# Performance work log

Hardware: AMD Instinct MI355X
Metric: run time of the kernel (lower is better)

The kernel has to match this reference:

```python
import jax, jax.numpy as jnp
import numpy as np

TOPK = 32
NUM_PT = 8192
NUM_KP = 8
HW = 19200


def _conv3(x, w, b):
    # x: [1, C, N], w: [O, C, 3] -> [1, O, N] (padding=1)
    y = jax.lax.conv_general_dilated(x, w, (1,), [(1, 1)],
                                     dimension_numbers=('NCH', 'OIH', 'NCH'))
    return y + b[None, :, None]


def setup_inputs() -> dict:
    key = jax.random.key(0)
    ks = jax.random.split(key, 64)

    def p(i, *shape):
        return (jax.random.normal(ks[i], shape, dtype=jnp.float32) * 0.05)

    inp = {
        'seg': jax.random.uniform(ks[0], (1, NUM_PT), dtype=jnp.float32),
        'img': jax.random.normal(ks[1], (1, 32, HW), dtype=jnp.float32),
        'cloud': jax.random.normal(ks[2], (1, NUM_PT, 3), dtype=jnp.float32),
        't': jax.random.normal(ks[3], (1, 3), dtype=jnp.float32),
        'choose': jax.random.randint(ks[4], (1, 1, NUM_PT), 0, HW),
        # Pseudo3DConv params (all 1x1 conv1d == channel matmul)
        'pconv1_w': p(5, 64, 3),    'pconv1_b': p(6, 64),
        'pconv2_w': p(7, 128, 64),  'pconv2_b': p(8, 128),
        'conv1_w': p(9, 64, 32),    'conv1_b': p(10, 64),
        'conv2_w': p(11, 128, 64),  'conv2_b': p(12, 128),
        'psconv1_w': p(13, 256, 128), 'psconv1_b': p(14, 256),
        'psconv2_w': p(15, 128, 256), 'psconv2_b': p(16, 128),
        'final_w': p(17, 128, 416), 'final_b': p(18, 128),
        # heads
        'seg1_w': p(19, 64, 128, 3), 'seg1_b': p(20, 64),
        'seg2_w': p(21, 32, 64),     'seg2_b': p(22, 32),
        'seg3_w': p(23, 1, 32),      'seg3_b': p(24, 1),
        'dis1_w': p(25, 64, 128, 3), 'dis1_b': p(26, 64),
        'dis2_w': p(27, 32, 64),     'dis2_b': p(28, 32),
        'dis3_w': p(29, 1, 32),      'dis3_b': p(30, 1),
        'lin1_w': p(31, 90, 128),    'lin1_b': p(32, 90),
        'lin2_w': p(33, 64, 90),     'lin2_b': p(34, 64),
        'lin3_w': p(35, 3 * NUM_KP, 64), 'lin3_b': p(36, 3 * NUM_KP),
    }
    return inp


def reference(seg, img, cloud, t, choose,
              pconv1_w, pconv1_b, pconv2_w, pconv2_b,
              conv1_w, conv1_b, conv2_w, conv2_b,
              psconv1_w, psconv1_b, psconv2_w, psconv2_b,
              final_w, final_b,
              seg1_w, seg1_b, seg2_w, seg2_b, seg3_w, seg3_b,
              dis1_w, dis1_b, dis2_w, dis2_b, dis3_w, dis3_b,
              lin1_w, lin1_b, lin2_w, lin2_b, lin3_w, lin3_b):
    lrelu = jax.nn.leaky_relu  # slope 0.01, same as torch default
    N = NUM_PT

    # gather per-point image features at chosen pixels: [N, 32]
    feat = jnp.take(img[0], choose[0, 0], axis=1).T
    c = cloud[0]  # [N, 3]

    # ---- KNN (self included, as in knn_cuda) ----
    d2 = jnp.sum((c[:, None, :] - c[None, :, :]) ** 2, axis=-1)  # [N, N]
    _, idx = jax.lax.top_k(-d2, TOPK)  # [N, K] nearest neighbors

    # ---- point-feature MLP (pconv1 -> lrelu -> pconv2) ----
    pf = lrelu(c @ pconv1_w.T + pconv1_b) @ pconv2_w.T + pconv2_b  # [N, 128]

    # ---- vectorized per-point neighbor gather + MLP + weighted maxpool ----
    nf = feat[idx]    # [N, K, 32]
    npf = pf[idx]     # [N, K, 128]
    npos = c[idx]     # [N, K, 3]
    w = jax.nn.softmax(-jnp.linalg.norm(c[:, None, :] - npos, axis=-1), axis=1)  # [N, K]

    f = lrelu(nf @ conv1_w.T + conv1_b) @ conv2_w.T + conv2_b          # [N, K, 128]
    fp = lrelu(npf @ psconv1_w.T + psconv1_b) @ psconv2_w.T + psconv2_b  # [N, K, 128]
    f = jnp.max(f * w[..., None], axis=1)    # [N, 128]
    fp = jnp.max(fp * w[..., None], axis=1)  # [N, 128]

    # final2 = [fp | img_feat], final1 = [f | cloud_feat] -> cat -> [N, 416]
    final = jnp.concatenate([fp, feat, f, pf], axis=1)
    fused = lrelu(final) @ final_w.T + final_b  # [N, 128]
    fused = fused.T[None]  # [1, 128, N]

    def pw(x, w_, b_):  # 1x1 conv1d on [1, C, N]
        return jnp.einsum('oc,bcn->bon', w_, x) + b_[None, :, None]

    # segmentation head
    h = lrelu(_conv3(fused, seg1_w, seg1_b))
    seg_pre = pw(lrelu(pw(h, seg2_w, seg2_b)), seg3_w, seg3_b).reshape(1, N)

    # distance-to-center weighting (norm along coord dim, softmax over points)
    dis_center = jax.nn.softmax(
        jnp.linalg.norm(cloud - (-t)[:, None, :], axis=2), axis=1)  # [1, N]

    # distance head (on unweighted fused features, matching torch op order)
    h = lrelu(_conv3(fused, dis1_w, dis1_b))
    dis_pre = pw(lrelu(pw(h, dis2_w, dis2_b)), dis3_w, dis3_b).reshape(1, N)

    # weight fused features by center distance and segmentation, sum-pool
    fused = fused * dis_center[:, None, :] * seg[:, None, :]
    g = jnp.sum(fused, axis=2)  # [1, 128]

    kp = lrelu(g @ lin1_w.T + lin1_b)
    kp = lrelu(kp @ lin2_w.T + lin2_b)
    keypoints = (kp @ lin3_w.T + lin3_b).reshape(1, NUM_KP, 3)
    return keypoints, dis_pre, dis_center, seg_pre
```

## Files before the change

### kernel.cpp

```cpp
#include <hip/hip_runtime.h>
#include <math.h>

#define NPT 8192
#define HWIMG 19200
#define KCAP 128

using short8 = __attribute__((ext_vector_type(8))) short;
using short4v = __attribute__((ext_vector_type(4))) short;
using f32x4  = __attribute__((ext_vector_type(4))) float;

__device__ __forceinline__ float lrelu(float x) { return x > 0.f ? x : 0.01f * x; }
__device__ __forceinline__ unsigned short f2bf(float v) {
  unsigned u = __float_as_uint(v);
  return (unsigned short)((u + 0x7fffu + ((u >> 16) & 1u)) >> 16);
}
__device__ __forceinline__ float bf2f(unsigned short h) {
  return __uint_as_float(((unsigned)h) << 16);
}
__device__ __forceinline__ void split2(float v, unsigned short& h, unsigned short& l) {
  h = f2bf(v);
  l = f2bf(v - bf2f(h));
}
__device__ __forceinline__ void mfma3(f32x4& acc, short8 ah, short8 al, short8 wh, short8 wl) {
  acc = __builtin_amdgcn_mfma_f32_16x16x32_bf16(ah, wh, acc, 0, 0, 0);
  acc = __builtin_amdgcn_mfma_f32_16x16x32_bf16(al, wh, acc, 0, 0, 0);
  acc = __builtin_amdgcn_mfma_f32_16x16x32_bf16(ah, wl, acc, 0, 0, 0);
}

__device__ __forceinline__ int swz(int o, int k, int Kc) {
  return ((((o >> 4) * Kc + (k >> 5)) << 6) + (((k >> 3) & 3) << 4) + (o & 15)) * 8 + (k & 7);
}

#define OFF_PCONV2  0
#define OFF_CONV1   8192
#define OFF_CONV2   10240
#define OFF_PSCONV1 18432
#define OFF_PSCONV2 51200
#define OFF_FINAL   83968
#define OFF_W3      137216
#define OFF_W2P     186368

#define S_C4    NPT
#define S_G     129
#define S_BIASC 128
#define S_B2C   64
#define S_FEAT  (NPT*32)
#define S_W3    49152
#define S_W2P   8192
#define S_WSPL  OFF_W3
#define PREP_TOTAL (S_C4 + S_G + S_BIASC + S_B2C + S_FEAT + S_W3 + S_W2P + S_WSPL)
__global__ void k_prep(const float* __restrict__ cloud, const int* __restrict__ choose,
                       const float* __restrict__ img,
                       const float* __restrict__ seg1_w, const float* __restrict__ dis1_w,
                       const float* __restrict__ seg1_b, const float* __restrict__ dis1_b,
                       const float* __restrict__ seg2_w, const float* __restrict__ dis2_w,
                       const float* __restrict__ seg2_b, const float* __restrict__ dis2_b,
                       const float* __restrict__ pconv2_w, const float* __restrict__ conv1_w,
                       const float* __restrict__ conv2_w, const float* __restrict__ psconv1_w,
                       const float* __restrict__ psconv2_w, const float* __restrict__ final_w,
                       float* __restrict__ c4, float* __restrict__ g,
                       float* __restrict__ biasc, float* __restrict__ bias2c,
                       float* __restrict__ feat,
                       unsigned short* __restrict__ feat_h, unsigned short* __restrict__ feat_l,
                       unsigned short* __restrict__ Wh, unsigned short* __restrict__ Wl) {
  int j = blockIdx.x * blockDim.x + threadIdx.x;
  if (j < S_C4) {
    float x = cloud[j*3+0], y = cloud[j*3+1], z = cloud[j*3+2];
    float4 v; v.x = x; v.y = y; v.z = z; v.w = x*x + y*y + z*z;
    ((float4*)c4)[j] = v;
    return;
  }
  j -= S_C4;
  if (j < S_G) { g[j] = 0.f; return; }
  j -= S_G;
  if (j < S_BIASC) { biasc[j] = (j < 64) ? seg1_b[j] : dis1_b[j-64]; return; }
  j -= S_BIASC;
  if (j < S_B2C) { bias2c[j] = (j < 32) ? seg2_b[j] : dis2_b[j-32]; return; }
  j -= S_B2C;
  if (j < S_FEAT) {
    int n = j >> 5, ch = j & 31;
    float v = img[ch*HWIMG + choose[n]];
    feat[j] = v;
    unsigned short hh, ll; split2(v, hh, ll);
    int d = swz(n, ch, 1);
    feat_h[d] = hh; feat_l[d] = ll;
    return;
  }
  j -= S_FEAT;
  if (j < S_W3) {
    int h = j / 24576, r = j - h*24576, o = r / 384, k = r - o*384;
    int t = k >> 7, c = k & 127;
    float v = (h ? dis1_w : seg1_w)[o*384 + c*3 + t];
    unsigned short hh, ll; split2(v, hh, ll);
    int d = OFF_W3 + swz(h*64 + o, k, 12);
    Wh[d] = hh; Wl[d] = ll;
    return;
  }
  j -= S_W3;
  if (j < S_W2P) {
    int o = j >> 7, c = j & 127;
    float v = 0.f;
    if (o < 32) { if (c < 64) v = seg2_w[o*64 + c]; }
    else        { if (c >= 64) v = dis2_w[(o-32)*64 + (c-64)]; }
    unsigned short hh, ll; split2(v, hh, ll);
    int d = OFF_W2P + swz(o, c, 4);
    Wh[d] = hh; Wl[d] = ll;
    return;
  }
  j -= S_W2P;
  if (j < S_WSPL) {
    float v; int d;
    if (j < OFF_CONV1) {
      int o = j >> 6, k = j & 63;
      v = pconv2_w[j]; d = OFF_PCONV2 + swz(o, k, 2);
    } else if (j < OFF_CONV2) {
      int jj = j - OFF_CONV1, o = jj >> 5, k = jj & 31;
      v = conv1_w[jj]; d = OFF_CONV1 + swz(o, k, 1);
    } else if (j < OFF_PSCONV1) {
      int jj = j - OFF_CONV2, o = jj >> 6, k = jj & 63;
      v = conv2_w[jj]; d = OFF_CONV2 + swz(o, k, 2);
    } else if (j < OFF_PSCONV2) {
      int jj = j - OFF_PSCONV1, o = jj >> 7, k = jj & 127;
      v = psconv1_w[jj]; d = OFF_PSCONV1 + swz(o, k, 4);
    } else if (j < OFF_FINAL) {
      int jj = j - OFF_PSCONV2, o = jj >> 8, k = jj & 255;
      v = psconv2_w[jj]; d = OFF_PSCONV2 + swz(o, k, 8);
    } else {
      int jj = j - OFF_FINAL, o = jj / 416, k = jj - o*416;
      v = final_w[jj]; d = OFF_FINAL + swz(o, k, 13);
    }
    unsigned short hh, ll; split2(v, hh, ll);
    Wh[d] = hh; Wl[d] = ll;
  }
}

__device__ __forceinline__ unsigned bsort32u(unsigned key, int lane) {
#pragma unroll
  for (int k = 2; k <= 64; k <<= 1) {
#pragma unroll
    for (int j = k >> 1; j > 0; j >>= 1) {
      unsigned o = __shfl_xor(key, j, 64);
      bool keepmin = (((lane & j) == 0) == ((lane & k) == 0));
      key = ((o < key) == keepmin) ? o : key;
    }
  }
  return key;
}
__device__ __forceinline__ unsigned long long bsort64(unsigned long long key, int lane) {
#pragma unroll
  for (int k = 2; k <= 64; k <<= 1) {
#pragma unroll
    for (int j = k >> 1; j > 0; j >>= 1) {
      unsigned long long o = __shfl_xor(key, j, 64);
      bool keepmin = (((lane & j) == 0) == ((lane & k) == 0));
      bool omin = o < key;
      key = (omin == keepmin) ? o : key;
    }
  }
  return key;
}
__device__ __forceinline__ unsigned long long bmerge64(unsigned long long key, int lane) {
#pragma unroll
  for (int j = 32; j > 0; j >>= 1) {
    unsigned long long o = __shfl_xor(key, j, 64);
    bool keepmin = ((lane & j) == 0);
    bool omin = o < key;
    key = (omin == keepmin) ? o : key;
  }
  return key;
}

#define MEGA_GRID 3073
__global__ __launch_bounds__(256) void k_mega(const float4* __restrict__ c4,
                                              int* __restrict__ idxo, float* __restrict__ wo,
                                              const float* __restrict__ cloud,
                                              const float* __restrict__ tvec,
                                              float* __restrict__ dc,
                                              const float* __restrict__ pconv1_w, const float* __restrict__ pconv1_b,
                                              const float* __restrict__ pconv2_b, const float* __restrict__ psconv1_b,
                                              const float* __restrict__ psconv2_b,
                                              const unsigned short* __restrict__ feat_h,
                                              const unsigned short* __restrict__ feat_l,
                                              const float* __restrict__ conv1_b, const float* __restrict__ conv2_b,
                                              const unsigned short* __restrict__ Wh,
                                              const unsigned short* __restrict__ Wl,
                                              float* __restrict__ pf, float* __restrict__ Yfp,
                                              float* __restrict__ Yf) {
  __shared__ __align__(16) char smem[16384];
  int tid = threadIdx.x, lane = tid & 63, w = tid >> 6;
  int mr = lane & 15, q = lane >> 4;
  if (blockIdx.x > 2048) {
    unsigned short* sh_h = (unsigned short*)smem;
    unsigned short* sh_l = (unsigned short*)(smem + 8192);
    int cb = blockIdx.x - 2049;
    if (cb < 512) {
      int m0 = cb * 16;
      float4 cp = c4[m0 + mr];
      short8 ah0, al0, ah1, al1;
#pragma unroll
      for (int j = 0; j < 8; ++j) {
        int c0 = q*8 + j, c1 = 32 + q*8 + j;
        float v0 = lrelu(fmaf(cp.x, pconv1_w[c0*3+0], fmaf(cp.y, pconv1_w[c0*3+1],
                          fmaf(cp.z, pconv1_w[c0*3+2], pconv1_b[c0]))));
        float v1 = lrelu(fmaf(cp.x, pconv1_w[c1*3+0], fmaf(cp.y, pconv1_w[c1*3+1],
                          fmaf(cp.z, pconv1_w[c1*3+2], pconv1_b[c1]))));
        unsigned short hh, ll;
        split2(v0, hh, ll); ah0[j] = (short)hh; al0[j] = (short)ll;
        split2(v1, hh, ll); ah1[j] = (short)hh; al1[j] = (short)ll;
      }
      f32x4 acc[2];
#pragma unroll
      for (int t = 0; t < 2; ++t) { f32x4 z = {0.f,0.f,0.f,0.f}; acc[t] = z; }
      const unsigned short* W2h = Wh + OFF_PCONV2;
      const unsigned short* W2l = Wl + OFF_PCONV2;
#pragma unroll
      for (int tt = 0; tt < 2; ++tt) {
        int t1 = 2*w + tt;
        int w0 = ((t1*2 + 0)*64 + lane)*8, w1 = ((t1*2 + 1)*64 + lane)*8;
        mfma3(acc[tt], ah0, al0, *(const short8*)(W2h + w0), *(const short8*)(W2l + w0));
        mfma3(acc[tt], ah1, al1, *(const short8*)(W2h + w1), *(const short8*)(W2l + w1));
      }
#pragma unroll
      for (int tt = 0; tt < 2; ++tt) {
        int t1 = 2*w + tt, n = t1*16 + mr;
        float b = pconv2_b[n];
        int ks2 = t1 >> 1, q2 = (t1 & 1)*2 + (mr >> 3), jd = mr & 7;
#pragma unroll
        for (int r = 0; r < 4; ++r) {
          int row = q*4 + r;
          float v = acc[tt][r] + b;
          pf[(size_t)(m0+row)*128 + n] = v;
          unsigned short hh, ll; split2(v, hh, ll);
          int p = ((ks2*16 + row)*4 + q2)*8 + jd;
          sh_h[p] = hh; sh_l[p] = ll;
        }
      }
      __syncthreads();
      f32x4 acc3[2];
#pragma unroll
      for (int t = 0; t < 2; ++t) { f32x4 z = {0.f,0.f,0.f,0.f}; acc3[t] = z; }
      const unsigned short* W3h = Wh + OFF_PSCONV1;
      const unsigned short* W3l = Wl + OFF_PSCONV1;
      const unsigned short* W4h = Wh + OFF_PSCONV2;
      const unsigned short* W4l = Wl + OFF_PSCONV2;
#pragma unroll
      for (int h = 0; h < 2; ++h) {
        f32x4 acc2[2];
#pragma unroll
        for (int t = 0; t < 2; ++t) { f32x4 z = {0.f,0.f,0.f,0.f}; acc2[t] = z; }
#pragma unroll
        for (int ks = 0; ks < 4; ++ks) {
          int ap = ((ks*16 + mr)*4 + q)*8;
          short8 ah = *(const short8*)&sh_h[ap];
          short8 al = *(const short8*)&sh_l[ap];
#pragma unroll
          for (int tt = 0; tt < 2; ++tt) {
            int ts = h*8 + 2*w + tt;
            int wb = ((ts*4 + ks)*64 + lane)*8;
            mfma3(acc2[tt], ah, al, *(const short8*)(W3h + wb), *(const short8*)(W3l + wb));
          }
        }
#pragma unroll
        for (int tt = 0; tt < 2; ++tt) {
          int tl = 2*w + tt;
          int n = h*128 + tl*16 + mr;
          float b = psconv1_b[n];
          int ks3 = tl >> 1, q3 = (tl & 1)*2 + (mr >> 3), jd = mr & 7;
#pragma unroll
          for (int r = 0; r < 4; ++r) {
            int row = q*4 + r;
            float v = lrelu(acc2[tt][r] + b);
            unsigned short hh, ll; split2(v, hh, ll);
            int p = 2048 + ((ks3*16 + row)*4 + q3)*8 + jd;
            sh_h[p] = hh; sh_l[p] = ll;
          }
        }
        __syncthreads();
#pragma unroll
        for (int ks = 0; ks < 4; ++ks) {
          int ap = 2048 + ((ks*16 + mr)*4 + q)*8;
          short8 ah = *(const short8*)&sh_h[ap];
          short8 al = *(const short8*)&sh_l[ap];
#pragma unroll
          for (int tt = 0; tt < 2; ++tt) {
            int wb = (((2*w+tt)*8 + h*4 + ks)*64 + lane)*8;
            mfma3(acc3[tt], ah, al, *(const short8*)(W4h + wb), *(const short8*)(W4l + wb));
          }
        }
        __syncthreads();
      }
#pragma unroll
      for (int tt = 0; tt < 2; ++tt) {
        int n = (2*w+tt)*16 + mr;
        float b = psconv2_b[n];
#pragma unroll
        for (int r = 0; r < 4; ++r)
          Yfp[(size_t)(m0 + q*4 + r)*128 + n] = acc3[tt][r] + b;
      }
    } else {
      int m0 = (cb - 512) * 16;
      int ab = ((m0 >> 4)*64 + lane)*8;
      short8 ah = *(const short8*)(feat_h + ab);
      short8 al = *(const short8*)(feat_l + ab);
      f32x4 acc = {0.f,0.f,0.f,0.f};
      const unsigned short* W1h = Wh + OFF_CONV1;
      const unsigned short* W1l = Wl + OFF_CONV1;
      {
        int wb = (w*64 + lane)*8;
        mfma3(acc, ah, al, *(const short8*)(W1h + wb), *(const short8*)(W1l + wb));
      }
      {
        int n = w*16 + mr;
        float b = conv1_b[n];
        int ks2 = n >> 5, q2 = (n >> 3) & 3, jd = mr & 7;
#pragma unroll
        for (int r = 0; r < 4; ++r) {
          int row = q*4 + r;
          float v = lrelu(acc[r] + b);
          unsigned short hh, ll; split2(v, hh, ll);
          int p = ((ks2*16 + row)*4 + q2)*8 + jd;
          sh_h[p] = hh; sh_l[p] = ll;
        }
      }
      __syncthreads();
      f32x4 acc2[2];
#pragma unroll
      for (int t = 0; t < 2; ++t) { f32x4 z = {0.f,0.f,0.f,0.f}; acc2[t] = z; }
      const unsigned short* W2h = Wh + OFF_CONV2;
      const unsigned short* W2l = Wl + OFF_CONV2;
#pragma unroll
      for (int ks = 0; ks < 2; ++ks) {
        int ap = ((ks*16 + mr)*4 + q)*8;
        short8 a2 = *(const short8*)&sh_h[ap];
        short8 a2l = *(const short8*)&sh_l[ap];
#pragma unroll
        for (int tt = 0; tt < 2; ++tt) {
          int wb = (((2*w+tt)*2 + ks)*64 + lane)*8;
          mfma3(acc2[tt], a2, a2l, *(const short8*)(W2h + wb), *(const short8*)(W2l + wb));
        }
      }
#pragma unroll
      for (int tt = 0; tt < 2; ++tt) {
        int n = (2*w+tt)*16 + mr;
        float b = conv2_b[n];
#pragma unroll
        for (int r = 0; r < 4; ++r)
          Yf[(size_t)(m0 + q*4 + r)*128 + n] = acc2[tt][r] + b;
      }
    }
    return;
  }
  if (blockIdx.x == 2048) {
    float* sred = (float*)smem;
    float tx = tvec[0], ty = tvec[1], tz = tvec[2];
    float v[32];
    float m = -INFINITY;
#pragma unroll
    for (int i2 = 0; i2 < 32; ++i2) {
      int n = i2*256 + tid;
      float ax = cloud[n*3+0] + tx, ay = cloud[n*3+1] + ty, az = cloud[n*3+2] + tz;
      v[i2] = sqrtf(ax*ax + ay*ay + az*az);
      m = fmaxf(m, v[i2]);
    }
#pragma unroll
    for (int o = 1; o < 64; o <<= 1) m = fmaxf(m, __shfl_xor(m, o, 64));
    if (lane == 0) sred[w] = m;
    __syncthreads();
    m = fmaxf(fmaxf(sred[0], sred[1]), fmaxf(sred[2], sred[3]));
    __syncthreads();
    float s = 0.f;
#pragma unroll
    for (int i2 = 0; i2 < 32; ++i2) { v[i2] = expf(v[i2] - m); s += v[i2]; }
#pragma unroll
    for (int o = 1; o < 64; o <<= 1) s += __shfl_xor(s, o, 64);
    if (lane == 0) sred[w] = s;
    __syncthreads();
    s = sred[0] + sred[1] + sred[2] + sred[3];
#pragma unroll
    for (int i2 = 0; i2 < 32; ++i2) dc[i2*256 + tid] = v[i2] / s;
    return;
  }
  float (*smin)[256] = (float(*)[256])smem;
  float* sTv = (float*)(smem + 4096);
  int*   scnt = (int*)(smem + 4112);
  float (*sd)[KCAP] = (float(*)[KCAP])(smem + 4128);
  int   (*sj)[KCAP] = (int(*)[KCAP])(smem + 6176);
  int q0 = blockIdx.x * 4;
  float4 p0 = c4[q0], p1 = c4[q0+1], p2 = c4[q0+2], p3 = c4[q0+3];
  float p0x = -2.f*p0.x, p0y = -2.f*p0.y, p0z = -2.f*p0.z;
  float p1x = -2.f*p1.x, p1y = -2.f*p1.y, p1z = -2.f*p1.z;
  float p2x = -2.f*p2.x, p2y = -2.f*p2.y, p2z = -2.f*p2.z;
  float p3x = -2.f*p3.x, p3y = -2.f*p3.y, p3z = -2.f*p3.z;
#define DDOT(PX,PY,PZ,PW,CJ) fmaf(PX,(CJ).x, fmaf(PY,(CJ).y, fmaf(PZ,(CJ).z, PW + (CJ).w)))
  float m0 = INFINITY, m1 = INFINITY, m2 = INFINITY, m3 = INFINITY;
  for (int t = 0; t < 32; ++t) {
    float4 cj = c4[t*256 + tid];
    m0 = fminf(m0, DDOT(p0x,p0y,p0z,p0.w,cj));
    m1 = fminf(m1, DDOT(p1x,p1y,p1z,p1.w,cj));
    m2 = fminf(m2, DDOT(p2x,p2y,p2z,p2.w,cj));
    m3 = fminf(m3, DDOT(p3x,p3y,p3z,p3.w,cj));
  }
  smin[0][tid] = m0; smin[1][tid] = m1; smin[2][tid] = m2; smin[3][tid] = m3;
  if (tid < 4) scnt[tid] = 0;
  __syncthreads();
  {
    float4 vv = *(const float4*)&smin[w][lane*4];
    float m4 = fmaxf(fminf(fminf(vv.x, vv.y), fminf(vv.z, vv.w)), 0.f);
    unsigned key = bsort32u(__float_as_uint(m4), lane);
    float T = __uint_as_float(__shfl(key, 31, 64));
    if (lane == 0) sTv[w] = T * (1.f + 2e-5f) + 4e-5f;
  }
  __syncthreads();
  float T0 = sTv[0], T1 = sTv[1], T2 = sTv[2], T3 = sTv[3];
  for (int t = 0; t < 32; ++t) {
    int j = t*256 + tid;
    float4 cj = c4[j];
    float d;
#define APPEND(Q, P) { \
    float dx_ = (P).x-cj.x, dy_ = (P).y-cj.y, dz_ = (P).z-cj.z; \
    float de_ = dx_*dx_ + dy_*dy_ + dz_*dz_; \
    int p_ = atomicAdd(&scnt[Q],1); if (p_ < KCAP) { sd[Q][p_] = de_; sj[Q][p_] = j; } }
    d = DDOT(p0x,p0y,p0z,p0.w,cj); if (d <= T0) APPEND(0, p0);
    d = DDOT(p1x,p1y,p1z,p1.w,cj); if (d <= T1) APPEND(1, p1);
    d = DDOT(p2x,p2y,p2z,p2.w,cj); if (d <= T2) APPEND(2, p2);
    d = DDOT(p3x,p3y,p3z,p3.w,cj); if (d <= T3) APPEND(3, p3);
  }
  __syncthreads();
  int M = scnt[w]; if (M > KCAP) M = KCAP;
  unsigned long long key = (lane < M)
      ? (((unsigned long long)__float_as_uint(sd[w][lane]) << 32) | (unsigned)sj[w][lane])
      : ~0ull;
  key = bsort64(key, lane);
  for (int base = 64; base < M; base += 64) {
    unsigned long long nk = (base + lane < M)
        ? (((unsigned long long)__float_as_uint(sd[w][base+lane]) << 32) | (unsigned)sj[w][base+lane])
        : ~0ull;
    nk = bsort64(nk, lane);
    nk = __shfl_xor(nk, 63, 64);
    key = key < nk ? key : nk;
    key = bmerge64(key, lane);
  }
  float dsel = __uint_as_float((unsigned)(key >> 32));
  int   jsel = (int)(unsigned)(key & 0xffffffffu);
  float v = -sqrtf(dsel);
  float mx = v;
#pragma unroll
  for (int o = 1; o < 32; o <<= 1) mx = fmaxf(mx, __shfl_xor(mx, o, 64));
  float e = expf(v - mx);
  float s = e;
#pragma unroll
  for (int o = 1; o < 32; o <<= 1) s += __shfl_xor(s, o, 64);
  if (lane < 32) {
    int qd = q0 + w;
    wo[qd*32 + lane] = e / s;
    idxo[qd*32 + lane] = jsel;
  }
}

__global__ __launch_bounds__(256) void k_tail(const float* __restrict__ Yf,
                                              const float* __restrict__ Yfp,
                                              const float* __restrict__ feat,
                                              const float* __restrict__ pf,
                                              const int* __restrict__ idx,
                                              const float* __restrict__ wsm,
                                              const unsigned short* __restrict__ Wh,
                                              const unsigned short* __restrict__ Wl,
                                              const float* __restrict__ final_b,
                                              const float* __restrict__ biasc,
                                              const float* __restrict__ bias2c,
                                              const float* __restrict__ segw, const float* __restrict__ segb,
                                              const float* __restrict__ disw, const float* __restrict__ disb,
                                              unsigned short* __restrict__ fusedh,
                                              unsigned short* __restrict__ fusedl,
                                              float* __restrict__ osegp, float* __restrict__ odisp) {
  __shared__ int sjn[18][32];
  __shared__ float swn[18][32];
  __shared__ __align__(16) char sbuf[37440];
  int tid = threadIdx.x, lane = tid & 63, w = tid >> 6;
  int mr = lane & 15, q = lane >> 4;
  int mt = blockIdx.x, m0 = mt * 16;
  for (int t = tid; t < 18*32; t += 256) {
    int lr = t >> 5, k = t & 31, gr = m0 - 1 + lr;
    if (gr >= 0 && gr < NPT) { sjn[lr][k] = idx[gr*32+k]; swn[lr][k] = wsm[gr*32+k]; }
    else { sjn[lr][k] = 0; swn[lr][k] = 0.f; }
  }
  __syncthreads();
  for (int t = tid; t < 1872; t += 256) {
    int lr, col;
    float4 v4;
    if (t < 1152) {
      lr = t >> 6; int arr = (t >> 5) & 1, cg = t & 31;
      const float* Y = arr ? Yf : Yfp;
      float ax = -INFINITY, ay = -INFINITY, az = -INFINITY, aw = -INFINITY;
#pragma unroll 8
      for (int k = 0; k < 32; ++k) {
        float4 vv = *(const float4*)&Y[(size_t)sjn[lr][k]*128 + cg*4];
        float wk = swn[lr][k];
        ax = fmaxf(ax, wk*vv.x); ay = fmaxf(ay, wk*vv.y);
        az = fmaxf(az, wk*vv.z); aw = fmaxf(aw, wk*vv.w);
      }
      v4.x = lrelu(ax); v4.y = lrelu(ay); v4.z = lrelu(az); v4.w = lrelu(aw);
      col = (arr ? 160 : 0) + cg*4;
    } else if (t < 1728) {
      int u = t - 1152; lr = u >> 5; int cg = u & 31;
      int gr = m0 - 1 + lr;
      int gc = gr < 0 ? 0 : (gr >= NPT ? NPT-1 : gr);
      float4 p4 = *(const float4*)&pf[(size_t)gc*128 + cg*4];
      v4.x = lrelu(p4.x); v4.y = lrelu(p4.y); v4.z = lrelu(p4.z); v4.w = lrelu(p4.w);
      col = 288 + cg*4;
    } else {
      int u = t - 1728; lr = u >> 3; int cg = u & 7;
      int gr = m0 - 1 + lr;
      int gc = gr < 0 ? 0 : (gr >= NPT ? NPT-1 : gr);
      float4 p4 = *(const float4*)&feat[(size_t)gc*32 + cg*4];
      v4.x = lrelu(p4.x); v4.y = lrelu(p4.y); v4.z = lrelu(p4.z); v4.w = lrelu(p4.w);
      col = 128 + cg*4;
    }
    int gr = m0 - 1 + lr;
    if (gr < 0 || gr >= NPT) { v4.x = 0.f; v4.y = 0.f; v4.z = 0.f; v4.w = 0.f; }
    int ks = col >> 5, qq = (col >> 3) & 3, j0 = col & 7;
    char* base = sbuf + (ks*18 + lr)*80 + qq*16 + j0*2;
    short4v hv, lv;
    unsigned short hh, ll;
    split2(v4.x, hh, ll); hv[0] = (short)hh; lv[0] = (short)ll;
    split2(v4.y, hh, ll); hv[1] = (short)hh; lv[1] = (short)ll;
    split2(v4.z, hh, ll); hv[2] = (short)hh; lv[2] = (short)ll;
    split2(v4.w, hh, ll); hv[3] = (short)hh; lv[3] = (short)ll;
    *(short4v*)base = hv;
    *(short4v*)(base + 18720) = lv;
  }
  __syncthreads();
  f32x4 accA[2], accB[2];
#pragma unroll
  for (int t = 0; t < 2; ++t) {
    f32x4 z = {0.f,0.f,0.f,0.f}; accA[t] = z; accB[t] = z;
  }
  const unsigned short* WFh = Wh + OFF_FINAL;
  const unsigned short* WFl = Wl + OFF_FINAL;
#pragma unroll
  for (int ks = 0; ks < 13; ++ks) {
    int arB = 16 + mr; if (arB > 17) arB = 17;
    const char* pA = sbuf + (ks*18 + mr)*80 + q*16;
    const char* pB = sbuf + (ks*18 + arB)*80 + q*16;
    short8 ahA = *(const short8*)pA;
    short8 alA = *(const short8*)(pA + 18720);
    short8 ahB = *(const short8*)pB;
    short8 alB = *(const short8*)(pB + 18720);
#pragma unroll
    for (int tt = 0; tt < 2; ++tt) {
      int wb = (((2*w+tt)*13 + ks)*64 + lane)*8;
      short8 wh = *(const short8*)(WFh + wb);
      short8 wl = *(const short8*)(WFl + wb);
      mfma3(accA[tt], ahA, alA, wh, wl);
      mfma3(accB[tt], ahB, alB, wh, wl);
    }
  }
  __syncthreads();
#pragma unroll
  for (int tile = 0; tile < 2; ++tile) {
#pragma unroll
    for (int tt = 0; tt < 2; ++tt) {
      int t2 = 2*w + tt, n = t2*16 + mr;
      float b = final_b[n];
      int ksA = t2 >> 1, qq = (t2 & 1)*2 + (mr >> 3), jd = mr & 7;
#pragma unroll
      for (int r = 0; r < 4; ++r) {
        int lr = tile*16 + q*4 + r;
        if (lr > 17) continue;
        int gr = m0 - 1 + lr;
        float v = (tile ? accB[tt][r] : accA[tt][r]) + b;
        if (gr < 0 || gr >= NPT) v = 0.f;
        unsigned short hh, ll; split2(v, hh, ll);
        char* p = sbuf + (ksA*18 + lr)*80 + qq*16 + jd*2;
        *(unsigned short*)p = hh;
        *(unsigned short*)(p + 5760) = ll;
      }
    }
  }
  __syncthreads();
  {
    int ks2 = tid >> 6, q2 = (tid >> 4) & 3, mr2 = tid & 15;
    int lr = mr2 + 1;
    const char* p = sbuf + (ks2*18 + lr)*80 + q2*16;
    short8 oh = *(const short8*)p;
    short8 ol = *(const short8*)(p + 5760);
    size_t pos = ((size_t)mt*256 + tid)*8;
    *(short8*)(fusedh + pos) = oh;
    *(short8*)(fusedl + pos) = ol;
  }
  f32x4 acc3[2];
#pragma unroll
  for (int t = 0; t < 2; ++t) { f32x4 z = {0.f,0.f,0.f,0.f}; acc3[t] = z; }
  const unsigned short* W3h = Wh + OFF_W3;
  const unsigned short* W3l = Wl + OFF_W3;
#pragma unroll
  for (int ks = 0; ks < 12; ++ks) {
    int tap = ks >> 2, ksA = ks & 3;
    int ar = mr + tap;
    const char* p = sbuf + (ksA*18 + ar)*80 + q*16;
    short8 ah = *(const short8*)p;
    short8 al = *(const short8*)(p + 5760);
#pragma unroll
    for (int tt = 0; tt < 2; ++tt) {
      int wb = (((2*w+tt)*12 + ks)*64 + lane)*8;
      mfma3(acc3[tt], ah, al, *(const short8*)(W3h + wb), *(const short8*)(W3l + wb));
    }
  }
#pragma unroll
  for (int tt = 0; tt < 2; ++tt) {
    int t2 = 2*w + tt, n = t2*16 + mr;
    float b = biasc[n];
    int ks2 = t2 >> 1, q2 = (t2 & 1)*2 + (mr >> 3), jd = mr & 7;
#pragma unroll
    for (int r = 0; r < 4; ++r) {
      int row = q*4 + r;
      float v = lrelu(acc3[tt][r] + b);
      unsigned short hh, ll; split2(v, hh, ll);
      char* p = sbuf + 11520 + (ks2*16 + row)*80 + q2*16 + jd*2;
      *(unsigned short*)p = hh;
      *(unsigned short*)(p + 5120) = ll;
    }
  }
  __syncthreads();
  f32x4 acc4 = {0.f,0.f,0.f,0.f};
  const unsigned short* WPh = Wh + OFF_W2P;
  const unsigned short* WPl = Wl + OFF_W2P;
#pragma unroll
  for (int ks = 0; ks < 4; ++ks) {
    const char* p = sbuf + 11520 + (ks*16 + mr)*80 + q*16;
    short8 ah = *(const short8*)p;
    short8 al = *(const short8*)(p + 5120);
    int wb = ((w*4 + ks)*64 + lane)*8;
    mfma3(acc4, ah, al, *(const short8*)(WPh + wb), *(const short8*)(WPl + wb));
  }
  float hw = (w < 2) ? segw[w*16 + mr] : disw[(w-2)*16 + mr];
  float bb = bias2c[w*16 + mr];
  float* shead = (float*)(sbuf + 21760);
#pragma unroll
  for (int r = 0; r < 4; ++r)
    shead[(w*16 + q*4 + r)*17 + mr] = lrelu(acc4[r] + bb) * hw;
  __syncthreads();
  if (tid < 16) {
    float a = 0.f;
#pragma unroll
    for (int i = 0; i < 16; ++i) a += shead[(tid)*17 + i] + shead[(16 + tid)*17 + i];
    osegp[m0 + tid] = a + segb[0];
  } else if (tid < 32) {
    int r2 = tid - 16;
    float a = 0.f;
#pragma unroll
    for (int i = 0; i < 16; ++i) a += shead[(32 + r2)*17 + i] + shead[(48 + r2)*17 + i];
    odisp[m0 + r2] = a + disb[0];
  }
}

__global__ __launch_bounds__(256) void k_gk(const unsigned short* __restrict__ Ah,
                                            const unsigned short* __restrict__ Al,
                                            const float* __restrict__ dc,
                                            const float* __restrict__ seg,
                                            float* __restrict__ g,
                                            const float* __restrict__ l1w, const float* __restrict__ l1b,
                                            const float* __restrict__ l2w, const float* __restrict__ l2b,
                                            const float* __restrict__ l3w, const float* __restrict__ l3b,
                                            float* __restrict__ o_kp) {
  __shared__ float sred[2048];
  __shared__ int slast;
  int tid = threadIdx.x;
  int b = blockIdx.x;
  float pg[8] = {0.f,0.f,0.f,0.f,0.f,0.f,0.f,0.f};
  int mrr = tid & 15;
  for (int mi = 0; mi < 16; ++mi) {
    int m = b*16 + mi;
    int row = m*16 + mrr;
    float wrow = dc[row] * seg[row];
    size_t pos = ((size_t)m*256 + tid)*8;
    short8 hv = *(const short8*)(Ah + pos);
    short8 lv = *(const short8*)(Al + pos);
#pragma unroll
    for (int j = 0; j < 8; ++j)
      pg[j] += (bf2f((unsigned short)hv[j]) + bf2f((unsigned short)lv[j])) * wrow;
  }
#pragma unroll
  for (int j = 0; j < 8; ++j) sred[tid*8 + j] = pg[j];
  __syncthreads();
  if (tid < 128) {
    int ks = tid >> 5, q2 = (tid >> 3) & 3, j = tid & 7;
    float s = 0.f;
#pragma unroll
    for (int mr2 = 0; mr2 < 16; ++mr2) s += sred[((ks<<6) + (q2<<4) + mr2)*8 + j];
    atomicAdd(&g[tid], s);
  }
  __threadfence();
  __syncthreads();
  if (tid == 0) slast = (atomicAdd((int*)(g + 128), 1) == 31);
  __syncthreads();
  if (!slast) return;
  __shared__ float sg[128], s1[90], s2[64];
  if (tid < 128) sg[tid] = atomicAdd(&g[tid], 0.f);
  __syncthreads();
  if (tid < 90) {
    float a = l1b[tid];
    for (int i = 0; i < 128; ++i) a += sg[i]*l1w[tid*128+i];
    s1[tid] = lrelu(a);
  }
  __syncthreads();
  if (tid < 64) {
    float a = l2b[tid];
    for (int i = 0; i < 90; ++i) a += s1[i]*l2w[tid*90+i];
    s2[tid] = lrelu(a);
  }
  __syncthreads();
  if (tid < 24) {
    float a = l3b[tid];
    for (int i = 0; i < 64; ++i) a += s2[i]*l3w[tid*64+i];
    o_kp[tid] = a;
  }
}

extern "C" void kernel_launch(void* const* d_in, const int* in_sizes, int n_in,
                              void* d_out, int out_size, void* d_ws, size_t ws_size,
                              hipStream_t stream) {
  const float* seg      = (const float*)d_in[0];
  const float* img      = (const float*)d_in[1];
  const float* cloud    = (const float*)d_in[2];
  const float* tvec     = (const float*)d_in[3];
  const int*   choose   = (const int*)d_in[4];
  const float* pconv1_w = (const float*)d_in[5];
  const float* pconv1_b = (const float*)d_in[6];
  const float* pconv2_w = (const float*)d_in[7];
  const float* pconv2_b = (const float*)d_in[8];
  const float* conv1_w  = (const float*)d_in[9];
  const float* conv1_b  = (const float*)d_in[10];
  const float* conv2_w  = (const float*)d_in[11];
  const float* conv2_b  = (const float*)d_in[12];
  const float* psconv1_w= (const float*)d_in[13];
  const float* psconv1_b= (const float*)d_in[14];
  const float* psconv2_w= (const float*)d_in[15];
  const float* psconv2_b= (const float*)d_in[16];
  const float* final_w  = (const float*)d_in[17];
  const float* final_b  = (const float*)d_in[18];
  const float* seg1_w   = (const float*)d_in[19];
  const float* seg1_b   = (const float*)d_in[20];
  const float* seg2_w   = (const float*)d_in[21];
  const float* seg2_b   = (const float*)d_in[22];
  const float* seg3_w   = (const float*)d_in[23];
  const float* seg3_b   = (const float*)d_in[24];
  const float* dis1_w   = (const float*)d_in[25];
  const float* dis1_b   = (const float*)d_in[26];
  const float* dis2_w   = (const float*)d_in[27];
  const float* dis2_b   = (const float*)d_in[28];
  const float* dis3_w   = (const float*)d_in[29];
  const float* dis3_b   = (const float*)d_in[30];
  const float* lin1_w   = (const float*)d_in[31];
  const float* lin1_b   = (const float*)d_in[32];
  const float* lin2_w   = (const float*)d_in[33];
  const float* lin2_b   = (const float*)d_in[34];
  const float* lin3_w   = (const float*)d_in[35];
  const float* lin3_b   = (const float*)d_in[36];

  float* out = (float*)d_out;
  float* ws  = (float*)d_ws;

  float* c4     = ws + 0;
  float* feat   = ws + 32768;
  unsigned short* feat_h = (unsigned short*)(ws + 294912);
  unsigned short* feat_l = (unsigned short*)(ws + 425984);
  float* pf     = ws + 557056;
  float* Yf     = ws + 1605632;
  float* Yfp    = ws + 2654208;
  int*   idx    = (int*)(ws + 3702784);
  float* wsm    = ws + 3964928;
  unsigned short* fusedh = (unsigned short*)(ws + 8683520);
  unsigned short* fusedl = (unsigned short*)(ws + 9207808);
  unsigned short* Wh    = (unsigned short*)(ws + 9732096);
  unsigned short* Wl    = (unsigned short*)(ws + 9829376);
  float* biasc  = ws + 9926656;
  float* bias2c = ws + 9926784;
  float* g      = ws + 9926848;

  float* o_kp   = out;
  float* o_disp = out + 24;
  float* o_dc   = out + 8216;
  float* o_segp = out + 16408;

  k_prep<<<(PREP_TOTAL + 255)/256, 256, 0, stream>>>(
      cloud, choose, img, seg1_w, dis1_w, seg1_b, dis1_b,
      seg2_w, dis2_w, seg2_b, dis2_b,
      pconv2_w, conv1_w, conv2_w, psconv1_w, psconv2_w, final_w,
      c4, g, biasc, bias2c, feat, feat_h, feat_l, Wh, Wl);

  k_mega<<<MEGA_GRID, 256, 0, stream>>>(
      (const float4*)c4, idx, wsm, cloud, tvec, o_dc,
      pconv1_w, pconv1_b, pconv2_b, psconv1_b, psconv2_b,
      feat_h, feat_l, conv1_b, conv2_b, Wh, Wl, pf, Yfp, Yf);

  k_tail<<<512, 256, 0, stream>>>(
      Yf, Yfp, feat, pf, idx, wsm, Wh, Wl,
      final_b, biasc, bias2c, seg3_w, seg3_b, dis3_w, dis3_b,
      fusedh, fusedl, o_segp, o_disp);

  k_gk<<<32, 256, 0, stream>>>(fusedh, fusedl, o_dc, seg, g,
                               lin1_w, lin1_b, lin2_w, lin2_b, lin3_w, lin3_b, o_kp);

  (void)in_sizes; (void)n_in; (void)out_size; (void)ws_size;
}
```

Before: 230.0 us.

## Fuse image gather into consumers and fold weighted pooling into tail kernel

The separate precompute of gathered image features (fp32 plus bf16 hi/lo split) in the prep kernel is removed. The mega and tail kernels now gather from img via choose directly, and the mega kernel splits the values in shared memory. The tail kernel also computes the dc*seg weighted sum-pool from its shared fused tile and atomically adds partials into g, which removes the fused-feature global writes and the k_gk reduction pass. A single-block k_kp then runs the MLP. This cuts global memory traffic and one reduction kernel, in exchange for redundant scattered img gathers and many atomics.

```diff
diff --git a/kernel.cpp b/kernel.cpp
--- a/kernel.cpp
+++ b/kernel.cpp
@@ -26,7 +26,6 @@
   acc = __builtin_amdgcn_mfma_f32_16x16x32_bf16(al, wh, acc, 0, 0, 0);
   acc = __builtin_amdgcn_mfma_f32_16x16x32_bf16(ah, wl, acc, 0, 0, 0);
 }
-
 __device__ __forceinline__ int swz(int o, int k, int Kc) {
   return ((((o >> 4) * Kc + (k >> 5)) << 6) + (((k >> 3) & 3) << 4) + (o & 15)) * 8 + (k & 7);
 }
@@ -44,13 +43,11 @@
 #define S_G     129
 #define S_BIASC 128
 #define S_B2C   64
-#define S_FEAT  (NPT*32)
 #define S_W3    49152
 #define S_W2P   8192
 #define S_WSPL  OFF_W3
-#define PREP_TOTAL (S_C4 + S_G + S_BIASC + S_B2C + S_FEAT + S_W3 + S_W2P + S_WSPL)
-__global__ void k_prep(const float* __restrict__ cloud, const int* __restrict__ choose,
-                       const float* __restrict__ img,
+#define PREP_TOTAL (S_C4 + S_G + S_BIASC + S_B2C + S_W3 + S_W2P + S_WSPL)
+__global__ void k_prep(const float* __restrict__ cloud,
                        const float* __restrict__ seg1_w, const float* __restrict__ dis1_w,
                        const float* __restrict__ seg1_b, const float* __restrict__ dis1_b,
                        const float* __restrict__ seg2_w, const float* __restrict__ dis2_w,
@@ -60,8 +57,6 @@
                        const float* __restrict__ psconv2_w, const float* __restrict__ final_w,
                        float* __restrict__ c4, float* __restrict__ g,
                        float* __restrict__ biasc, float* __restrict__ bias2c,
-                       float* __restrict__ feat,
-                       unsigned short* __restrict__ feat_h, unsigned short* __restrict__ feat_l,
                        unsigned short* __restrict__ Wh, unsigned short* __restrict__ Wl) {
   int j = blockIdx.x * blockDim.x + threadIdx.x;
   if (j < S_C4) {
@@ -77,16 +72,6 @@
   j -= S_BIASC;
   if (j < S_B2C) { bias2c[j] = (j < 32) ? seg2_b[j] : dis2_b[j-32]; return; }
   j -= S_B2C;
-  if (j < S_FEAT) {
-    int n = j >> 5, ch = j & 31;
-    float v = img[ch*HWIMG + choose[n]];
-    feat[j] = v;
-    unsigned short hh, ll; split2(v, hh, ll);
-    int d = swz(n, ch, 1);
-    feat_h[d] = hh; feat_l[d] = ll;
-    return;
-  }
-  j -= S_FEAT;
   if (j < S_W3) {
     int h = j / 24576, r = j - h*24576, o = r / 384, k = r - o*384;
     int t = k >> 7, c = k & 127;
@@ -179,8 +164,7 @@
                                               const float* __restrict__ pconv1_w, const float* __restrict__ pconv1_b,
                                               const float* __restrict__ pconv2_b, const float* __restrict__ psconv1_b,
                                               const float* __restrict__ psconv2_b,
-                                              const unsigned short* __restrict__ feat_h,
-                                              const unsigned short* __restrict__ feat_l,
+                                              const float* __restrict__ img, const int* __restrict__ choose,
                                               const float* __restrict__ conv1_b, const float* __restrict__ conv2_b,
                                               const unsigned short* __restrict__ Wh,
                                               const unsigned short* __restrict__ Wl,
@@ -299,9 +283,16 @@
       }
     } else {
       int m0 = (cb - 512) * 16;
-      int ab = ((m0 >> 4)*64 + lane)*8;
-      short8 ah = *(const short8*)(feat_h + ab);
-      short8 al = *(const short8*)(feat_l + ab);
+      for (int t = tid; t < 512; t += 256) {
+        int rw = t >> 5, ch = t & 31;
+        float v = img[ch*HWIMG + choose[m0 + rw]];
+        unsigned short hh, ll; split2(v, hh, ll);
+        int p = 1024 + ((ch >> 3)*16 + rw)*8 + (ch & 7);
+        sh_h[p] = hh; sh_l[p] = ll;
+      }
+      __syncthreads();
+      short8 ah = *(const short8*)&sh_h[1024 + (q*16 + mr)*8];
+      short8 al = *(const short8*)&sh_l[1024 + (q*16 + mr)*8];
       f32x4 acc = {0.f,0.f,0.f,0.f};
       const unsigned short* W1h = Wh + OFF_CONV1;
       const unsigned short* W1l = Wl + OFF_CONV1;
@@ -309,6 +300,7 @@
         int wb = (w*64 + lane)*8;
         mfma3(acc, ah, al, *(const short8*)(W1h + wb), *(const short8*)(W1l + wb));
       }
+      __syncthreads();
       {
         int n = w*16 + mr;
         float b = conv1_b[n];
@@ -459,7 +451,8 @@
 
 __global__ __launch_bounds__(256) void k_tail(const float* __restrict__ Yf,
                                               const float* __restrict__ Yfp,
-                                              const float* __restrict__ feat,
+                                              const float* __restrict__ img,
+                                              const int* __restrict__ choose,
                                               const float* __restrict__ pf,
                                               const int* __restrict__ idx,
                                               const float* __restrict__ wsm,
@@ -470,8 +463,8 @@
                                               const float* __restrict__ bias2c,
                                               const float* __restrict__ segw, const float* __restrict__ segb,
                                               const float* __restrict__ disw, const float* __restrict__ disb,
-                                              unsigned short* __restrict__ fusedh,
-                                              unsigned short* __restrict__ fusedl,
+                                              const float* __restrict__ dc, const float* __restrict__ seg,
+                                              float* __restrict__ g,
                                               float* __restrict__ osegp, float* __restrict__ odisp) {
   __shared__ int sjn[18][32];
   __shared__ float swn[18][32];
@@ -512,8 +505,11 @@
       int u = t - 1728; lr = u >> 3; int cg = u & 7;
       int gr = m0 - 1 + lr;
       int gc = gr < 0 ? 0 : (gr >= NPT ? NPT-1 : gr);
-      float4 p4 = *(const float4*)&feat[(size_t)gc*32 + cg*4];
-      v4.x = lrelu(p4.x); v4.y = lrelu(p4.y); v4.z = lrelu(p4.z); v4.w = lrelu(p4.w);
+      int ix = choose[gc];
+      v4.x = lrelu(img[(cg*4+0)*HWIMG + ix]);
+      v4.y = lrelu(img[(cg*4+1)*HWIMG + ix]);
+      v4.z = lrelu(img[(cg*4+2)*HWIMG + ix]);
+      v4.w = lrelu(img[(cg*4+3)*HWIMG + ix]);
       col = 128 + cg*4;
     }
     int gr = m0 - 1 + lr;
@@ -530,6 +526,8 @@
     *(short4v*)(base + 18720) = lv;
   }
   __syncthreads();
+  float* dcseg = &swn[0][0];
+  if (tid < 16) dcseg[tid] = dc[m0 + tid] * seg[m0 + tid];
   f32x4 accA[2], accB[2];
 #pragma unroll
   for (int t = 0; t < 2; ++t) {
@@ -578,16 +576,6 @@
     }
   }
   __syncthreads();
-  {
-    int ks2 = tid >> 6, q2 = (tid >> 4) & 3, mr2 = tid & 15;
-    int lr = mr2 + 1;
-    const char* p = sbuf + (ks2*18 + lr)*80 + q2*16;
-    short8 oh = *(const short8*)p;
-    short8 ol = *(const short8*)(p + 5760);
-    size_t pos = ((size_t)mt*256 + tid)*8;
-    *(short8*)(fusedh + pos) = oh;
-    *(short8*)(fusedl + pos) = ol;
-  }
   f32x4 acc3[2];
 #pragma unroll
   for (int t = 0; t < 2; ++t) { f32x4 z = {0.f,0.f,0.f,0.f}; acc3[t] = z; }
@@ -641,62 +629,43 @@
     shead[(w*16 + q*4 + r)*17 + mr] = lrelu(acc4[r] + bb) * hw;
   __syncthreads();
   if (tid < 16) {
-    float a = 0.f;
-#pragma unroll
-    for (int i = 0; i < 16; ++i) a += shead[(tid)*17 + i] + shead[(16 + tid)*17 + i];
-    osegp[m0 + tid] = a + segb[0];
+    float s = 0.f;
+#pragma unroll
+    for (int i = 0; i < 16; ++i) s += shead[(tid)*17 + i] + shead[(16 + tid)*17 + i];
+    osegp[m0 + tid] = s + segb[0];
   } else if (tid < 32) {
     int r2 = tid - 16;
-    float a = 0.f;
-#pragma unroll
-    for (int i = 0; i < 16; ++i) a += shead[(32 + r2)*17 + i] + shead[(48 + r2)*17 + i];
-    odisp[m0 + r2] = a + disb[0];
-  }
-}
-
-__global__ __launch_bounds__(256) void k_gk(const unsigned short* __restrict__ Ah,
-                                            const unsigned short* __restrict__ Al,
-                                            const float* __restrict__ dc,
-                                            const float* __restrict__ seg,
-                                            float* __restrict__ g,
+    float s = 0.f;
+#pragma unroll
+    for (int i = 0; i < 16; ++i) s += shead[(32 + r2)*17 + i] + shead[(48 + r2)*17 + i];
+    odisp[m0 + r2] = s + disb[0];
+  }
+  {
+    float* gpart = (float*)(sbuf + 26112);
+    int c = tid & 127, half = tid >> 7;
+    int ksA = c >> 5, qq = (c >> 3) & 3, jd = c & 7;
+    float acc = 0.f;
+#pragma unroll
+    for (int r8 = 0; r8 < 8; ++r8) {
+      int row = half*8 + r8;
+      const char* p = sbuf + (ksA*18 + (row + 1))*80 + qq*16 + jd*2;
+      float v = bf2f(*(const unsigned short*)p) + bf2f(*(const unsigned short*)(p + 5760));
+      acc += v * dcseg[row];
+    }
+    gpart[tid] = acc;
+    __syncthreads();
+    if (tid < 128) atomicAdd(&g[tid], gpart[tid] + gpart[tid + 128]);
+  }
+}
+
+__global__ __launch_bounds__(128) void k_kp(const float* __restrict__ g,
                                             const float* __restrict__ l1w, const float* __restrict__ l1b,
                                             const float* __restrict__ l2w, const float* __restrict__ l2b,
                                             const float* __restrict__ l3w, const float* __restrict__ l3b,
-                                            float* __restrict__ o_kp) {
-  __shared__ float sred[2048];
-  __shared__ int slast;
+                                            float* __restrict__ outp) {
+  __shared__ float sg[128], s1[90], s2[64];
   int tid = threadIdx.x;
-  int b = blockIdx.x;
-  float pg[8] = {0.f,0.f,0.f,0.f,0.f,0.f,0.f,0.f};
-  int mrr = tid & 15;
-  for (int mi = 0; mi < 16; ++mi) {
-    int m = b*16 + mi;
-    int row = m*16 + mrr;
-    float wrow = dc[row] * seg[row];
-    size_t pos = ((size_t)m*256 + tid)*8;
-    short8 hv = *(const short8*)(Ah + pos);
-    short8 lv = *(const short8*)(Al + pos);
-#pragma unroll
-    for (int j = 0; j < 8; ++j)
-      pg[j] += (bf2f((unsigned short)hv[j]) + bf2f((unsigned short)lv[j])) * wrow;
-  }
-#pragma unroll
-  for (int j = 0; j < 8; ++j) sred[tid*8 + j] = pg[j];
-  __syncthreads();
-  if (tid < 128) {
-    int ks = tid >> 5, q2 = (tid >> 3) & 3, j = tid & 7;
-    float s = 0.f;
-#pragma unroll
-    for (int mr2 = 0; mr2 < 16; ++mr2) s += sred[((ks<<6) + (q2<<4) + mr2)*8 + j];
-    atomicAdd(&g[tid], s);
-  }
-  __threadfence();
-  __syncthreads();
-  if (tid == 0) slast = (atomicAdd((int*)(g + 128), 1) == 31);
-  __syncthreads();
-  if (!slast) return;
-  __shared__ float sg[128], s1[90], s2[64];
-  if (tid < 128) sg[tid] = atomicAdd(&g[tid], 0.f);
+  sg[tid] = g[tid];
   __syncthreads();
   if (tid < 90) {
     float a = l1b[tid];
@@ -713,7 +682,7 @@
   if (tid < 24) {
     float a = l3b[tid];
     for (int i = 0; i < 64; ++i) a += s2[i]*l3w[tid*64+i];
-    o_kp[tid] = a;
+    outp[tid] = a;
   }
 }
 
@@ -762,21 +731,16 @@
   float* ws  = (float*)d_ws;
 
   float* c4     = ws + 0;
-  float* feat   = ws + 32768;
-  unsigned short* feat_h = (unsigned short*)(ws + 294912);
-  unsigned short* feat_l = (unsigned short*)(ws + 425984);
-  float* pf     = ws + 557056;
-  float* Yf     = ws + 1605632;
-  float* Yfp    = ws + 2654208;
-  int*   idx    = (int*)(ws + 3702784);
-  float* wsm    = ws + 3964928;
-  unsigned short* fusedh = (unsigned short*)(ws + 8683520);
-  unsigned short* fusedl = (unsigned short*)(ws + 9207808);
-  unsigned short* Wh    = (unsigned short*)(ws + 9732096);
-  unsigned short* Wl    = (unsigned short*)(ws + 9829376);
-  float* biasc  = ws + 9926656;
-  float* bias2c = ws + 9926784;
-  float* g      = ws + 9926848;
+  float* pf     = ws + 32768;
+  float* Yf     = ws + 1081344;
+  float* Yfp    = ws + 2129920;
+  int*   idx    = (int*)(ws + 3178496);
+  float* wsm    = ws + 3440640;
+  unsigned short* Wh = (unsigned short*)(ws + 3702784);
+  unsigned short* Wl = (unsigned short*)(ws + 3800064);
+  float* biasc  = ws + 3897344;
+  float* bias2c = ws + 3897472;
+  float* g      = ws + 3897536;
 
   float* o_kp   = out;
   float* o_disp = out + 24;
@@ -784,23 +748,22 @@
   float* o_segp = out + 16408;
 
   k_prep<<<(PREP_TOTAL + 255)/256, 256, 0, stream>>>(
-      cloud, choose, img, seg1_w, dis1_w, seg1_b, dis1_b,
+      cloud, seg1_w, dis1_w, seg1_b, dis1_b,
       seg2_w, dis2_w, seg2_b, dis2_b,
       pconv2_w, conv1_w, conv2_w, psconv1_w, psconv2_w, final_w,
-      c4, g, biasc, bias2c, feat, feat_h, feat_l, Wh, Wl);
+      c4, g, biasc, bias2c, Wh, Wl);
 
   k_mega<<<MEGA_GRID, 256, 0, stream>>>(
       (const float4*)c4, idx, wsm, cloud, tvec, o_dc,
       pconv1_w, pconv1_b, pconv2_b, psconv1_b, psconv2_b,
-      feat_h, feat_l, conv1_b, conv2_b, Wh, Wl, pf, Yfp, Yf);
+      img, choose, conv1_b, conv2_b, Wh, Wl, pf, Yfp, Yf);
 
   k_tail<<<512, 256, 0, stream>>>(
-      Yf, Yfp, feat, pf, idx, wsm, Wh, Wl,
+      Yf, Yfp, img, choose, pf, idx, wsm, Wh, Wl,
       final_b, biasc, bias2c, seg3_w, seg3_b, dis3_w, dis3_b,
-      fusedh, fusedl, o_segp, o_disp);
-
-  k_gk<<<32, 256, 0, stream>>>(fusedh, fusedl, o_dc, seg, g,
-                               lin1_w, lin1_b, lin2_w, lin2_b, lin3_w, lin3_b, o_kp);
+      o_dc, seg, g, o_segp, o_disp);
+
+  k_kp<<<1, 128, 0, stream>>>(g, lin1_w, lin1_b, lin2_w, lin2_b, lin3_w, lin3_b, o_kp);
 
   (void)in_sizes; (void)n_in; (void)out_size; (void)ws_size;
 }
```

New measurement: 236.2 us. 2.7% more time.
